# Kernel tuning notes

Measured on AMD Instinct MI355X. Metric: run time of the kernel, lower is better.

The kernel has to match this reference:

```python
import jax, jax.numpy as jnp
import numpy as np

N, E, F_IN = 100000, 3200000, 512
H1, D1, C = 8, 8, 16  # layer1 heads, per-head dim; layer2 out classes
NEG_SLOPE = 0.2


def _segment_softmax(e, dst, num_segments):
    # numerically-stable softmax over edges grouped by destination node
    m = jax.ops.segment_max(e, dst, num_segments=num_segments)
    ex = jnp.exp(e - m[dst])
    s = jax.ops.segment_sum(ex, dst, num_segments=num_segments)
    return ex / (s[dst] + 1e-16)


def _gat_layer(x, src, dst, W, a_src, a_dst, heads, d_out):
    n = x.shape[0]
    h = (x @ W).reshape(n, heads, d_out)          # [N,H,D]
    al_s = jnp.einsum('nhd,hd->nh', h, a_src)     # [N,H]
    al_d = jnp.einsum('nhd,hd->nh', h, a_dst)
    e = jax.nn.leaky_relu(al_s[src] + al_d[dst], NEG_SLOPE)  # [E,H]
    alpha = _segment_softmax(e, dst, n)           # [E,H]
    msg = h[src] * alpha[..., None]               # [E,H,D]
    return jax.ops.segment_sum(msg, dst, num_segments=n)  # [N,H,D]


def setup_inputs() -> dict:
    key = jax.random.key(0)
    ks = jax.random.split(key, 8)
    x = jax.random.normal(ks[0], (N, F_IN), dtype=jnp.float32)
    edge_index = jax.random.randint(ks[1], (2, E), 0, N, dtype=jnp.int64)
    W1 = jax.random.normal(ks[2], (F_IN, H1 * D1), dtype=jnp.float32) * (1.0 / np.sqrt(F_IN))
    a1_src = jax.random.normal(ks[3], (H1, D1), dtype=jnp.float32)
    a1_dst = jax.random.normal(ks[4], (H1, D1), dtype=jnp.float32)
    W2 = jax.random.normal(ks[5], (H1 * D1, C), dtype=jnp.float32) * (1.0 / np.sqrt(H1 * D1))
    a2_src = jax.random.normal(ks[6], (1, C), dtype=jnp.float32)
    a2_dst = jax.random.normal(ks[7], (1, C), dtype=jnp.float32)
    return {'x': x, 'edge_index': edge_index, 'W1': W1, 'a1_src': a1_src,
            'a1_dst': a1_dst, 'W2': W2, 'a2_src': a2_src, 'a2_dst': a2_dst}


def reference(x, edge_index, W1, a1_src, a1_dst, W2, a2_src, a2_dst):
    src, dst = edge_index[0], edge_index[1]
    # layer 1: 8 heads, concat, then ELU (dropout is identity in eval mode)
    h1 = _gat_layer(x, src, dst, W1, a1_src, a1_dst, H1, D1)  # [N,H1,D1]
    h1 = jax.nn.elu(h1.reshape(N, H1 * D1))                   # [N,64]
    # layer 2: single head -> class logits
    h2 = _gat_layer(h1, src, dst, W2, a2_src, a2_dst, 1, C)   # [N,1,C]
    return jax.nn.log_softmax(h2.reshape(N, C), axis=1)
```

## Files before the change

### kernel.cpp

```cpp
#include <hip/hip_runtime.h>
#include <math.h>

#define NEG 0.2f

typedef __attribute__((ext_vector_type(8))) short bf16x8;
typedef __attribute__((ext_vector_type(4))) float f32x4;

static __device__ __forceinline__ float lrelu(float x){ return x > 0.f ? x : NEG*x; }

static __device__ __forceinline__ void bsplit(float v, unsigned int& hi, unsigned int& lo){
  unsigned int u = __float_as_uint(v);
  unsigned int hb = (u + 0x7fffu + ((u >> 16) & 1u)) & 0xffff0000u;
  float hf = __uint_as_float(hb);
  float l = v - hf;
  unsigned int ul = __float_as_uint(l);
  hi = hb >> 16;
  lo = (ul + 0x7fffu + ((ul >> 16) & 1u)) >> 16;
}

static __device__ __forceinline__ float bf2f(unsigned short u){
  return __uint_as_float(((unsigned int)u) << 16);
}
static __device__ __forceinline__ unsigned short f2bf(float v){
  unsigned int u = __float_as_uint(v);
  return (unsigned short)((u + 0x7fffu + ((u >> 16) & 1u)) >> 16);
}

__global__ void k_zero(int* __restrict__ p, int n){
  int i = blockIdx.x*blockDim.x + threadIdx.x;
  if (i < n) p[i] = 0;
}

__global__ void k_flag(const int* __restrict__ u, int* __restrict__ flag){
  if (threadIdx.x == 0 && blockIdx.x == 0) {
    int z = 1;
    for (int e = 0; e < 64; ++e) if (u[2*e+1] != 0) { z = 0; break; }
    *flag = z;
  }
}

__global__ void k_count(const int* __restrict__ u, const int* __restrict__ flag,
                        int* __restrict__ cnt, int E){
  int e = blockIdx.x*blockDim.x + threadIdx.x;
  if (e >= E) return;
  int dst = (*flag) ? u[2*(E+e)] : u[E+e];
  atomicAdd(&cnt[dst], 1);
}

__global__ __launch_bounds__(256) void k_scan1(const int* __restrict__ cnt,
    int* __restrict__ ro, int* __restrict__ bsum, int n){
  int t = threadIdx.x;
  int base = blockIdx.x*1024 + t*4;
  int v0 = (base+0 < n) ? cnt[base+0] : 0;
  int v1 = (base+1 < n) ? cnt[base+1] : 0;
  int v2 = (base+2 < n) ? cnt[base+2] : 0;
  int v3 = (base+3 < n) ? cnt[base+3] : 0;
  int s = v0+v1+v2+v3;
  int lane = t & 63, w = t >> 6;
  int inc = s;
  for (int off = 1; off < 64; off <<= 1) {
    int tm = __shfl_up(inc, off);
    if (lane >= off) inc += tm;
  }
  __shared__ int wsum[4];
  if (lane == 63) wsum[w] = inc;
  __syncthreads();
  int wpre = 0;
  for (int k = 0; k < 4; ++k) if (k < w) wpre += wsum[k];
  int run = wpre + inc - s;
  if (base+0 < n) ro[base+0] = run; run += v0;
  if (base+1 < n) ro[base+1] = run; run += v1;
  if (base+2 < n) ro[base+2] = run; run += v2;
  if (base+3 < n) ro[base+3] = run; run += v3;
  if (t == 255) bsum[blockIdx.x] = run;
}

__global__ void k_scan2(int* __restrict__ bsum, int nb){
  int lane = threadIdx.x;
  int carry = 0;
  for (int b = 0; b < nb; b += 64) {
    int i = b + lane;
    int v = (i < nb) ? bsum[i] : 0;
    int inc = v;
    for (int off = 1; off < 64; off <<= 1) {
      int t = __shfl_up(inc, off);
      if (lane >= off) inc += t;
    }
    if (i < nb) bsum[i] = carry + inc - v;
    carry += __shfl(inc, 63);
  }
}

__global__ void k_scan3(int* __restrict__ ro, int* __restrict__ cur,
                        const int* __restrict__ bsum, int n, int E){
  int i = blockIdx.x*blockDim.x + threadIdx.x;
  if (i < n) {
    int v = ro[i] + bsum[i >> 10];
    ro[i] = v; cur[i] = v;
  }
  if (i == 0) ro[n] = E;
}

__global__ __launch_bounds__(256) void k_fill(const int* __restrict__ u,
    const int* __restrict__ flag, int* __restrict__ cur, int* __restrict__ csr,
    int E, int n){
  const int xcd = blockIdx.x & 7;
  const int sub = blockIdx.x >> 3;
  const int nsub = gridDim.x >> 3;
  const int lo = (int)(((long long)xcd * n) >> 3);
  const int hi = (int)(((long long)(xcd + 1) * n) >> 3);
  const long long e0 = ((long long)sub * E) / nsub;
  const long long e1 = ((long long)(sub + 1) * E) / nsub;
  const bool f = (*flag) != 0;
  for (long long e = e0 + threadIdx.x; e < e1; e += 256) {
    int dst = f ? u[2*(E + e)] : u[E + e];
    if (dst >= lo && dst < hi) {
      int src = f ? u[2*e] : u[e];
      int p = atomicAdd(&cur[dst], 1);
      csr[p] = src;
    }
  }
}

__global__ void k_wprep(const float* __restrict__ W1, unsigned short* __restrict__ wtH,
                        unsigned short* __restrict__ wtL){
  int i = blockIdx.x*256 + threadIdx.x;
  if (i >= 512*64) return;
  int k = i >> 6, c = i & 63;
  unsigned int hi, lo;
  bsplit(W1[i], hi, lo);
  wtH[c*512 + k] = (unsigned short)hi;
  wtL[c*512 + k] = (unsigned short)lo;
}

__global__ __launch_bounds__(256, 3) void k_proj1(const float* __restrict__ x,
    const unsigned short* __restrict__ wtH, const unsigned short* __restrict__ wtL,
    const float* __restrict__ a1s_g, const float* __restrict__ a1d_g,
    unsigned short* __restrict__ h1bf, float* __restrict__ al1s, float* __restrict__ al1d, int n){
  __shared__ unsigned short lds[24576];
  char* const ldsb = (char*)lds;
  const int tid = threadIdx.x;
  const int lane = tid & 63;
  const int w = tid >> 6;
  const int l16 = lane & 15;
  const int lhi = lane >> 4;
  const int n0 = blockIdx.x * 128;

  float as_c[4], ad_c[4];
  #pragma unroll
  for (int f = 0; f < 4; ++f) { as_c[f] = a1s_g[16*f + l16]; ad_c[f] = a1d_g[16*f + l16]; }

  f32x4 acc[2][4];
  #pragma unroll
  for (int m = 0; m < 2; ++m)
    #pragma unroll
    for (int f = 0; f < 4; ++f) acc[m][f] = (f32x4){0.f,0.f,0.f,0.f};

  for (int k0 = 0; k0 < 512; k0 += 64) {
    #pragma unroll
    for (int i = 0; i < 8; ++i) {
      int f4 = tid + i*256;
      int row = f4 >> 4;
      int k4 = f4 & 15;
      int node = n0 + row; if (node >= n) node = n - 1;
      float4 v = *(const float4*)&x[(size_t)node*512 + k0 + k4*4];
      unsigned int h0,h1_,h2,h3,l0,l1,l2,l3;
      bsplit(v.x, h0, l0); bsplit(v.y, h1_, l1);
      bsplit(v.z, h2, l2); bsplit(v.w, h3, l3);
      uint2 hp = make_uint2(h0 | (h1_<<16), h2 | (h3<<16));
      uint2 lp = make_uint2(l0 | (l1<<16),  l2 | (l3<<16));
      int byteoff = (row*128 + k4*8) ^ ((row & 7) << 4);
      *(uint2*)(ldsb + byteoff)         = hp;
      *(uint2*)(ldsb + 16384 + byteoff) = lp;
    }
    #pragma unroll
    for (int i = 0; i < 2; ++i) {
      int f8 = tid + i*256;
      int c = f8 >> 3;
      int kb = f8 & 7;
      uint4 hv = *(const uint4*)&wtH[c*512 + k0 + kb*8];
      uint4 lv = *(const uint4*)&wtL[c*512 + k0 + kb*8];
      int byteoff = (c*128 + kb*16) ^ ((c & 7) << 4);
      *(uint4*)(ldsb + 32768 + byteoff) = hv;
      *(uint4*)(ldsb + 40960 + byteoff) = lv;
    }
    __syncthreads();

    #pragma unroll
    for (int kk = 0; kk < 64; kk += 32) {
      bf16x8 ah[2], al_[2], bh[4], bl[4];
      #pragma unroll
      for (int m = 0; m < 2; ++m) {
        int row = 32*w + 16*m + l16;
        int byteoff = (row*128 + (kk + 8*lhi)*2) ^ ((row & 7) << 4);
        ah[m]  = *(const bf16x8*)(ldsb + byteoff);
        al_[m] = *(const bf16x8*)(ldsb + 16384 + byteoff);
      }
      #pragma unroll
      for (int f = 0; f < 4; ++f) {
        int c = 16*f + l16;
        int byteoff = (c*128 + (kk + 8*lhi)*2) ^ ((c & 7) << 4);
        bh[f] = *(const bf16x8*)(ldsb + 32768 + byteoff);
        bl[f] = *(const bf16x8*)(ldsb + 40960 + byteoff);
      }
      #pragma unroll
      for (int m = 0; m < 2; ++m)
        #pragma unroll
        for (int f = 0; f < 4; ++f) {
          acc[m][f] = __builtin_amdgcn_mfma_f32_16x16x32_bf16(ah[m],  bh[f], acc[m][f], 0, 0, 0);
          acc[m][f] = __builtin_amdgcn_mfma_f32_16x16x32_bf16(ah[m],  bl[f], acc[m][f], 0, 0, 0);
          acc[m][f] = __builtin_amdgcn_mfma_f32_16x16x32_bf16(al_[m], bh[f], acc[m][f], 0, 0, 0);
        }
    }
    __syncthreads();
  }

  #pragma unroll
  for (int m = 0; m < 2; ++m) {
    #pragma unroll
    for (int r = 0; r < 4; ++r) {
      int node = n0 + 32*w + 16*m + 4*lhi + r;
      bool ok = (node < n);
      #pragma unroll
      for (int f = 0; f < 4; ++f) {
        float v = acc[m][f][r];
        if (ok) h1bf[(size_t)node*64 + 16*f + l16] = f2bf(v);
        float vs = v * as_c[f], vd = v * ad_c[f];
        vs += __shfl_xor(vs, 1); vs += __shfl_xor(vs, 2); vs += __shfl_xor(vs, 4);
        vd += __shfl_xor(vd, 1); vd += __shfl_xor(vd, 2); vd += __shfl_xor(vd, 4);
        if (ok && (l16 & 7) == 0) {
          int head = 2*f + (l16 >> 3);
          al1s[node*8 + head] = vs;
          al1d[node*8 + head] = vd;
        }
      }
    }
  }
}

__global__ __launch_bounds__(256) void k_agg1(const int* __restrict__ ro,
    const int* __restrict__ csr, const float* __restrict__ al1s,
    const float* __restrict__ al1d, const unsigned short* __restrict__ h1bf,
    float* __restrict__ h1b, int n){
  int wid = blockIdx.x*4 + (threadIdx.x >> 6);
  if (wid >= n) return;
  int node = __builtin_amdgcn_readfirstlane(wid);
  int lane = threadIdx.x & 63;
  int h = lane >> 3;
  int beg = ro[node], end = ro[node+1];
  float ald = al1d[node*8 + h];
  float s = 0.f, acc = 0.f;
  if (beg < end) {
    int   srcb[4];
    float alb[4], hvb[4];
    #pragma unroll
    for (int j = 0; j < 4; ++j) {
      int idx = beg + j;
      srcb[j] = csr[idx < end ? idx : beg];
    }
    #pragma unroll
    for (int j = 0; j < 4; ++j) {
      alb[j] = al1s[srcb[j]*8 + h];
      hvb[j] = bf2f(h1bf[(size_t)srcb[j]*64 + lane]);
    }
    for (int t = beg; t < end; t += 4) {
      int   nsrc[4];
      float nal[4], nhv[4];
      #pragma unroll
      for (int j = 0; j < 4; ++j) {
        int idx = t + 4 + j;
        nsrc[j] = csr[idx < end ? idx : beg];
      }
      #pragma unroll
      for (int j = 0; j < 4; ++j) {
        nal[j] = al1s[nsrc[j]*8 + h];
        nhv[j] = bf2f(h1bf[(size_t)nsrc[j]*64 + lane]);
      }
      #pragma unroll
      for (int j = 0; j < 4; ++j) {
        float e = alb[j] + ald;
        e = e > 0.f ? e : NEG*e;
        float ex = (t + j < end) ? __expf(e) : 0.f;
        s += ex;
        acc = fmaf(hvb[j], ex, acc);
      }
      #pragma unroll
      for (int j = 0; j < 4; ++j) { srcb[j] = nsrc[j]; alb[j] = nal[j]; hvb[j] = nhv[j]; }
    }
  }
  float v = acc / (s + 1e-16f);
  v = v > 0.f ? v : expm1f(v);
  h1b[(size_t)node*64 + lane] = v;
}

__global__ __launch_bounds__(256) void k_proj2(const float* __restrict__ h1b,
    const float* __restrict__ W2, const float* __restrict__ a2s_g, const float* __restrict__ a2d_g,
    unsigned short* __restrict__ h2bf, float* __restrict__ al2s, float* __restrict__ al2d, int n){
  __shared__ float w[64*16];
  __shared__ float a2sv[16], a2dv[16];
  for (int i = threadIdx.x; i < 1024; i += 256) w[i] = W2[i];
  if (threadIdx.x < 16) { a2sv[threadIdx.x] = a2s_g[threadIdx.x]; a2dv[threadIdx.x] = a2d_g[threadIdx.x]; }
  __syncthreads();
  int c = threadIdx.x & 15;
  int nid = blockIdx.x*16 + (threadIdx.x >> 4);
  if (nid >= n) return;
  const float* row = h1b + (size_t)nid*64;
  float acc = 0.f;
  #pragma unroll
  for (int k0 = 0; k0 < 64; k0 += 4) {
    float4 r = *(const float4*)(row + k0);
    acc = fmaf(r.x, w[(k0+0)*16 + c], acc);
    acc = fmaf(r.y, w[(k0+1)*16 + c], acc);
    acc = fmaf(r.z, w[(k0+2)*16 + c], acc);
    acc = fmaf(r.w, w[(k0+3)*16 + c], acc);
  }
  h2bf[(size_t)nid*16 + c] = f2bf(acc);
  float vs = acc * a2sv[c], vd = acc * a2dv[c];
  vs += __shfl_xor(vs, 1); vs += __shfl_xor(vs, 2); vs += __shfl_xor(vs, 4); vs += __shfl_xor(vs, 8);
  vd += __shfl_xor(vd, 1); vd += __shfl_xor(vd, 2); vd += __shfl_xor(vd, 4); vd += __shfl_xor(vd, 8);
  if (c == 0) { al2s[nid] = vs; al2d[nid] = vd; }
}

__global__ __launch_bounds__(256) void k_agg2(const int* __restrict__ ro,
    const int* __restrict__ csr, const float* __restrict__ al2s,
    const float* __restrict__ al2d, const unsigned short* __restrict__ h2bf,
    float* __restrict__ out, int n){
  int wid = blockIdx.x*4 + (threadIdx.x >> 6);
  if (wid >= n) return;
  int node = __builtin_amdgcn_readfirstlane(wid);
  int lane = threadIdx.x & 63;
  int j = lane >> 4, c = lane & 15;
  int beg = ro[node], end = ro[node+1];
  float ald = al2d[node];
  float sp = 0.f, acc = 0.f;
  if (beg < end) {
    int i = beg + j;
    int sA = csr[i < end ? i : beg];
    float aA = al2s[sA];
    float hA = bf2f(h2bf[(size_t)sA*16 + c]);
    for (; i < end; i += 4) {
      int i2 = i + 4;
      int sB = csr[i2 < end ? i2 : beg];
      float aB = al2s[sB];
      float hB = bf2f(h2bf[(size_t)sB*16 + c]);
      float e = lrelu(aA + ald);
      float ex = __expf(e);
      sp += ex;
      acc = fmaf(ex, hA, acc);
      sA = sB; aA = aB; hA = hB;
    }
  }
  sp  += __shfl_xor(sp, 16);  sp  += __shfl_xor(sp, 32);
  acc += __shfl_xor(acc, 16); acc += __shfl_xor(acc, 32);
  float v = acc / (sp + 1e-16f);
  float mx = v;
  mx = fmaxf(mx, __shfl_xor(mx, 1)); mx = fmaxf(mx, __shfl_xor(mx, 2));
  mx = fmaxf(mx, __shfl_xor(mx, 4)); mx = fmaxf(mx, __shfl_xor(mx, 8));
  float l = v - mx;
  float se = __expf(l);
  se += __shfl_xor(se, 1); se += __shfl_xor(se, 2);
  se += __shfl_xor(se, 4); se += __shfl_xor(se, 8);
  float res = l - logf(se);
  if (j == 0) out[(size_t)node*16 + c] = res;
}

static inline size_t alignup(size_t x){ return (x + 255) & ~(size_t)255; }

extern "C" void kernel_launch(void* const* d_in, const int* in_sizes, int n_in,
                              void* d_out, int out_size, void* d_ws, size_t ws_size,
                              hipStream_t stream){
  const float* x   = (const float*)d_in[0];
  const int*   ei  = (const int*)  d_in[1];
  const float* W1  = (const float*)d_in[2];
  const float* a1s = (const float*)d_in[3];
  const float* a1d = (const float*)d_in[4];
  const float* W2  = (const float*)d_in[5];
  const float* a2s = (const float*)d_in[6];
  const float* a2d = (const float*)d_in[7];
  float* out = (float*)d_out;

  const int n = in_sizes[0] / 512;
  const int E = in_sizes[1] / 2;

  char* w = (char*)d_ws;
  unsigned short* h1bf = (unsigned short*)w; w += alignup((size_t)n*64*2);
  float* h1b  = (float*)w; w += alignup((size_t)n*64*4);
  float* al1s_ = (float*)w; w += alignup((size_t)n*8*4);
  float* al1d_ = (float*)w; w += alignup((size_t)n*8*4);
  unsigned short* h2bf = (unsigned short*)w; w += alignup((size_t)n*16*2);
  float* al2s_ = (float*)w; w += alignup((size_t)n*4);
  float* al2d_ = (float*)w; w += alignup((size_t)n*4);
  int* cnt    = (int*)w;   w += alignup((size_t)n*4);
  int* ro     = (int*)w;   w += alignup((size_t)(n+1)*4);
  int* cur    = (int*)w;   w += alignup((size_t)n*4);
  int* csr    = (int*)w;   w += alignup((size_t)E*4);
  int* bsum   = (int*)w;   w += alignup(512*4);
  int* flag   = (int*)w;   w += alignup(64);
  unsigned short* wtH = (unsigned short*)w; w += alignup(512*64*2);
  unsigned short* wtL = (unsigned short*)w; w += alignup(512*64*2);

  const int nb_scan = (n + 1023) / 1024;

  k_zero<<<(n+255)/256, 256, 0, stream>>>(cnt, n);
  k_flag<<<1, 64, 0, stream>>>(ei, flag);
  k_wprep<<<128, 256, 0, stream>>>(W1, wtH, wtL);
  k_count<<<(E+255)/256, 256, 0, stream>>>(ei, flag, cnt, E);
  k_scan1<<<nb_scan, 256, 0, stream>>>(cnt, ro, bsum, n);
  k_scan2<<<1, 64, 0, stream>>>(bsum, nb_scan);
  k_scan3<<<(n+255)/256, 256, 0, stream>>>(ro, cur, bsum, n, E);
  k_fill<<<2048, 256, 0, stream>>>(ei, flag, cur, csr, E, n);

  k_proj1<<<(n+127)/128, 256, 0, stream>>>(x, wtH, wtL, a1s, a1d, h1bf, al1s_, al1d_, n);
  k_agg1<<<(n+3)/4, 256, 0, stream>>>(ro, csr, al1s_, al1d_, h1bf, h1b, n);
  k_proj2<<<(n+15)/16, 256, 0, stream>>>(h1b, W2, a2s, a2d, h2bf, al2s_, al2d_, n);
  k_agg2<<<(n+3)/4, 256, 0, stream>>>(ro, csr, al2s_, al2d_, h2bf, out, n);
}
```

Before: 587.5 us.

## Load projection operands directly from global into registers, dropping LDS staging

```diff
diff --git a/kernel.cpp b/kernel.cpp
--- a/kernel.cpp
+++ b/kernel.cpp
@@ -24,6 +24,17 @@
 static __device__ __forceinline__ unsigned short f2bf(float v){
   unsigned int u = __float_as_uint(v);
   return (unsigned short)((u + 0x7fffu + ((u >> 16) & 1u)) >> 16);
+}
+
+static __device__ __forceinline__ void split8(float4 v0, float4 v1, bf16x8& h, bf16x8& l){
+  float vv[8] = {v0.x, v0.y, v0.z, v0.w, v1.x, v1.y, v1.z, v1.w};
+  #pragma unroll
+  for (int i = 0; i < 8; ++i) {
+    unsigned int hi, lo;
+    bsplit(vv[i], hi, lo);
+    h[i] = (short)hi;
+    l[i] = (short)lo;
+  }
 }
 
 __global__ void k_zero(int* __restrict__ p, int n){
@@ -137,14 +148,12 @@
     const unsigned short* __restrict__ wtH, const unsigned short* __restrict__ wtL,
     const float* __restrict__ a1s_g, const float* __restrict__ a1d_g,
     unsigned short* __restrict__ h1bf, float* __restrict__ al1s, float* __restrict__ al1d, int n){
-  __shared__ unsigned short lds[24576];
-  char* const ldsb = (char*)lds;
   const int tid = threadIdx.x;
   const int lane = tid & 63;
   const int w = tid >> 6;
   const int l16 = lane & 15;
   const int lhi = lane >> 4;
-  const int n0 = blockIdx.x * 128;
+  const int r0 = blockIdx.x*128 + w*32;
 
   float as_c[4], ad_c[4];
   #pragma unroll
@@ -156,70 +165,43 @@
     #pragma unroll
     for (int f = 0; f < 4; ++f) acc[m][f] = (f32x4){0.f,0.f,0.f,0.f};
 
-  for (int k0 = 0; k0 < 512; k0 += 64) {
-    #pragma unroll
-    for (int i = 0; i < 8; ++i) {
-      int f4 = tid + i*256;
-      int row = f4 >> 4;
-      int k4 = f4 & 15;
-      int node = n0 + row; if (node >= n) node = n - 1;
-      float4 v = *(const float4*)&x[(size_t)node*512 + k0 + k4*4];
-      unsigned int h0,h1_,h2,h3,l0,l1,l2,l3;
-      bsplit(v.x, h0, l0); bsplit(v.y, h1_, l1);
-      bsplit(v.z, h2, l2); bsplit(v.w, h3, l3);
-      uint2 hp = make_uint2(h0 | (h1_<<16), h2 | (h3<<16));
-      uint2 lp = make_uint2(l0 | (l1<<16),  l2 | (l3<<16));
-      int byteoff = (row*128 + k4*8) ^ ((row & 7) << 4);
-      *(uint2*)(ldsb + byteoff)         = hp;
-      *(uint2*)(ldsb + 16384 + byteoff) = lp;
-    }
-    #pragma unroll
-    for (int i = 0; i < 2; ++i) {
-      int f8 = tid + i*256;
-      int c = f8 >> 3;
-      int kb = f8 & 7;
-      uint4 hv = *(const uint4*)&wtH[c*512 + k0 + kb*8];
-      uint4 lv = *(const uint4*)&wtL[c*512 + k0 + kb*8];
-      int byteoff = (c*128 + kb*16) ^ ((c & 7) << 4);
-      *(uint4*)(ldsb + 32768 + byteoff) = hv;
-      *(uint4*)(ldsb + 40960 + byteoff) = lv;
-    }
-    __syncthreads();
-
-    #pragma unroll
-    for (int kk = 0; kk < 64; kk += 32) {
-      bf16x8 ah[2], al_[2], bh[4], bl[4];
-      #pragma unroll
-      for (int m = 0; m < 2; ++m) {
-        int row = 32*w + 16*m + l16;
-        int byteoff = (row*128 + (kk + 8*lhi)*2) ^ ((row & 7) << 4);
-        ah[m]  = *(const bf16x8*)(ldsb + byteoff);
-        al_[m] = *(const bf16x8*)(ldsb + 16384 + byteoff);
-      }
-      #pragma unroll
-      for (int f = 0; f < 4; ++f) {
-        int c = 16*f + l16;
-        int byteoff = (c*128 + (kk + 8*lhi)*2) ^ ((c & 7) << 4);
-        bh[f] = *(const bf16x8*)(ldsb + 32768 + byteoff);
-        bl[f] = *(const bf16x8*)(ldsb + 40960 + byteoff);
-      }
-      #pragma unroll
-      for (int m = 0; m < 2; ++m)
-        #pragma unroll
-        for (int f = 0; f < 4; ++f) {
-          acc[m][f] = __builtin_amdgcn_mfma_f32_16x16x32_bf16(ah[m],  bh[f], acc[m][f], 0, 0, 0);
-          acc[m][f] = __builtin_amdgcn_mfma_f32_16x16x32_bf16(ah[m],  bl[f], acc[m][f], 0, 0, 0);
-          acc[m][f] = __builtin_amdgcn_mfma_f32_16x16x32_bf16(al_[m], bh[f], acc[m][f], 0, 0, 0);
-        }
-    }
-    __syncthreads();
+  int rowA = r0 + l16;        if (rowA >= n) rowA = n - 1;
+  int rowB = r0 + 16 + l16;   if (rowB >= n) rowB = n - 1;
+  const float* xA = x + (size_t)rowA*512 + 8*lhi;
+  const float* xB = x + (size_t)rowB*512 + 8*lhi;
+  const unsigned short* wHp = wtH + (size_t)l16*512 + 8*lhi;
+  const unsigned short* wLp = wtL + (size_t)l16*512 + 8*lhi;
+
+  for (int k0 = 0; k0 < 512; k0 += 32) {
+    float4 a0 = *(const float4*)(xA + k0);
+    float4 a1v = *(const float4*)(xA + k0 + 4);
+    float4 b0 = *(const float4*)(xB + k0);
+    float4 b1v = *(const float4*)(xB + k0 + 4);
+    bf16x8 bh[4], bl[4];
+    #pragma unroll
+    for (int f = 0; f < 4; ++f) {
+      bh[f] = *(const bf16x8*)(wHp + (size_t)f*16*512 + k0);
+      bl[f] = *(const bf16x8*)(wLp + (size_t)f*16*512 + k0);
+    }
+    bf16x8 ahA, alA, ahB, alB;
+    split8(a0, a1v, ahA, alA);
+    split8(b0, b1v, ahB, alB);
+    #pragma unroll
+    for (int f = 0; f < 4; ++f) {
+      acc[0][f] = __builtin_amdgcn_mfma_f32_16x16x32_bf16(ahA, bh[f], acc[0][f], 0, 0, 0);
+      acc[0][f] = __builtin_amdgcn_mfma_f32_16x16x32_bf16(ahA, bl[f], acc[0][f], 0, 0, 0);
+      acc[0][f] = __builtin_amdgcn_mfma_f32_16x16x32_bf16(alA, bh[f], acc[0][f], 0, 0, 0);
+      acc[1][f] = __builtin_amdgcn_mfma_f32_16x16x32_bf16(ahB, bh[f], acc[1][f], 0, 0, 0);
+      acc[1][f] = __builtin_amdgcn_mfma_f32_16x16x32_bf16(ahB, bl[f], acc[1][f], 0, 0, 0);
+      acc[1][f] = __builtin_amdgcn_mfma_f32_16x16x32_bf16(alB, bh[f], acc[1][f], 0, 0, 0);
+    }
   }
 
   #pragma unroll
   for (int m = 0; m < 2; ++m) {
     #pragma unroll
     for (int r = 0; r < 4; ++r) {
-      int node = n0 + 32*w + 16*m + 4*lhi + r;
+      int node = r0 + 16*m + 4*lhi + r;
       bool ok = (node < n);
       #pragma unroll
       for (int f = 0; f < 4; ++f) {
```

Measured after the change: 582.8 us. No clear change (-0.8%).
